# Performance work log

Hardware: AMD Instinct MI355X
Metric: run time of the kernel (lower is better)

## Reference

```python
import jax, jax.numpy as jnp
import numpy as np

EPS = 1e-10

def _quantize_one(x, codebook):
    # x: [B, T, D]; codebook: [K, D]
    B, T, D = x.shape
    K = codebook.shape[0]
    flat = x.reshape(-1, D)  # [N, D]
    # squared euclidean distance (argmin of this == argmax of -dist in torch code)
    dist = (jnp.sum(flat * flat, axis=-1, keepdims=True)
            - 2.0 * flat @ codebook.T
            + jnp.sum(codebook * codebook, axis=-1))  # [N, K]
    ind = jnp.argmin(dist, axis=-1)  # [N]
    q = codebook[ind].reshape(B, T, D)
    # commitment loss: mse(quantize.detach(), x) * commitment(=1.0)
    loss = jnp.mean((jax.lax.stop_gradient(q) - x) ** 2)
    # straight-through estimator
    q_st = x + jax.lax.stop_gradient(q - x)
    # perplexity from one-hot encodings
    counts = jnp.zeros((K,), dtype=x.dtype).at[ind].add(1.0)
    avg_probs = counts / ind.shape[0]
    perplexity = jnp.exp(-jnp.sum(avg_probs * jnp.log(avg_probs + EPS)))
    return q_st, loss, perplexity

def setup_inputs() -> dict:
    key = jax.random.key(0)
    k1, k2 = jax.random.split(key)
    z = jax.random.normal(k1, (16, 64, 4096), dtype=jnp.float32)
    codebooks = jax.random.normal(k2, (8, 1024, 64), dtype=jnp.float32)
    return {"z": z, "codebooks": codebooks}

def reference(z, codebooks):
    # z: [B, code_dim, T] -> transpose(2,1) -> [B, T, code_dim]
    x = jnp.transpose(z, (0, 2, 1))

    def step(carry, cb):
        residual, quantized_out = carry
        q, loss, perp = _quantize_one(residual, cb)
        return (residual - q, quantized_out + q), (loss, perp)

    (_, quantized_out), (losses, perplexities) = jax.lax.scan(
        step, (x, jnp.zeros_like(x)), codebooks)
    zq = jnp.transpose(quantized_out, (0, 2, 1))  # back to [B, code_dim, T]
    return zq, losses, perplexities
```

## Files before the change

kernel.cpp:

```cpp
#include <hip/hip_runtime.h>

#define S      8
#define K      1024
#define D      64
#define NVEC   65536
#define NW     2048
#define NELEM  4194304.0f
#define EPSQ   1e-10f
#define DELTA  0.005f

typedef __attribute__((ext_vector_type(8))) short  short8;
typedef __attribute__((ext_vector_type(4))) float  float4v;

static __device__ inline unsigned short f2bf(float f) {
    unsigned int u = __float_as_uint(f);
    u = (u + 0x7FFFu + ((u >> 16) & 1u)) >> 16;
    return (unsigned short)u;
}
static __device__ inline float bf2f(unsigned short h) {
    return __uint_as_float(((unsigned int)h) << 16);
}

__global__ void rvq_prep(const float* __restrict__ cb,
                         unsigned short* __restrict__ cbi,
                         float* __restrict__ c2, unsigned* __restrict__ cnt) {
    int i = blockIdx.x * blockDim.x + threadIdx.x;
    if (i < S * K) {
        const float* row = cb + (size_t)i * D;
        float a0 = 0.f, a1 = 0.f, a2 = 0.f, a3 = 0.f;
#pragma unroll
        for (int d = 0; d < D; d += 4) {
            a0 = fmaf(row[d+0], row[d+0], a0);
            a1 = fmaf(row[d+1], row[d+1], a1);
            a2 = fmaf(row[d+2], row[d+2], a2);
            a3 = fmaf(row[d+3], row[d+3], a3);
        }
        c2[i] = (a0 + a1) + (a2 + a3);
        cnt[i] = 0u;
    }
    int s  = i >> 12;
    int tau = (i >> 6) & 63;
    int l  = i & 63;
    int m  = l & 15, qq = l >> 4;
    const float* row = cb + (size_t)(s * K + tau * 16 + m) * D;
    short8 h0h, h0l, h1h, h1l;
#pragma unroll
    for (int e = 0; e < 8; ++e) {
        float x = row[qq * 8 + e];
        unsigned short h = f2bf(x);
        h0h[e] = (short)h; h0l[e] = (short)f2bf(x - bf2f(h));
        float y = row[32 + qq * 8 + e];
        unsigned short g = f2bf(y);
        h1h[e] = (short)g; h1l[e] = (short)f2bf(y - bf2f(g));
    }
    unsigned short* rec = cbi + (size_t)(s * 64 + tau) * 2048 + l * 8;
    *(short8*)(rec +    0) = h0h;
    *(short8*)(rec +  512) = h1h;
    *(short8*)(rec + 1024) = h0l;
    *(short8*)(rec + 1536) = h1l;
}

__global__ __launch_bounds__(64, 2)
void rvq_main(const float* __restrict__ z, const float* __restrict__ cbf,
              const unsigned short* __restrict__ cbi,
              const float* __restrict__ c2, float* __restrict__ zq,
              float* __restrict__ lossp, unsigned* __restrict__ cnt) {
    const int lane = threadIdx.x;
    const int m    = lane & 15;
    const int q    = lane >> 4;
    const int wid  = blockIdx.x;
    const int vbase = wid * 32;
    const int b    = vbase >> 12;
    const int ta   = (vbase & 4095) + m;
    const int tb   = ta + 16;
    const size_t zrow = ((size_t)(b * 64)) << 12;

    float ra0[8], ra1[8], rb0[8], rb1[8];
#pragma unroll
    for (int i = 0; i < 8; ++i) {
        ra0[i] = z[zrow + ((size_t)(q*8+i)    << 12) + ta];
        ra1[i] = z[zrow + ((size_t)(32+q*8+i) << 12) + ta];
        rb0[i] = z[zrow + ((size_t)(q*8+i)    << 12) + tb];
        rb1[i] = z[zrow + ((size_t)(32+q*8+i) << 12) + tb];
    }

#define LOADTILE(B0v, B1v, B2v, B3v, CCv, tt) {                              \
        const unsigned short* p_ = recs + (size_t)(tt) * 2048 + lane * 8;    \
        B0v = *(const short8*)(p_);                                          \
        B1v = *(const short8*)(p_ + 512);                                    \
        B2v = *(const short8*)(p_ + 1024);                                   \
        B3v = *(const short8*)(p_ + 1536);                                   \
        CCv = c2s[(tt) * 16 + m]; }

#pragma unroll 1
    for (int s = 0; s < S; ++s) {
        short8 xa0h, xa0l, xa1h, xa1l, xb0h, xb0l, xb1h, xb1l;
#pragma unroll
        for (int i = 0; i < 8; ++i) {
            unsigned short h;
            h = f2bf(ra0[i]); xa0h[i] = (short)h; xa0l[i] = (short)f2bf(ra0[i] - bf2f(h));
            h = f2bf(ra1[i]); xa1h[i] = (short)h; xa1l[i] = (short)f2bf(ra1[i] - bf2f(h));
            h = f2bf(rb0[i]); xb0h[i] = (short)h; xb0l[i] = (short)f2bf(rb0[i] - bf2f(h));
            h = f2bf(rb1[i]); xb1h[i] = (short)h; xb1l[i] = (short)f2bf(rb1[i] - bf2f(h));
        }

        float b1a[4], b2a[4], b1b[4], b2b[4];
        int   k1a[4], k1b[4];
#pragma unroll
        for (int j = 0; j < 4; ++j) {
            b1a[j] = 3.4e38f; b2a[j] = 3.4e38f; k1a[j] = 0;
            b1b[j] = 3.4e38f; b2b[j] = 3.4e38f; k1b[j] = 0;
        }

        const unsigned short* recs = cbi + (size_t)s * 131072;
        const float*          c2s  = c2 + s * K;

        short8 A0, A1, A2, A3, C0, C1, C2, C3;
        float  ca, cb2;
        LOADTILE(A0, A1, A2, A3, ca,  0);
        LOADTILE(C0, C1, C2, C3, cb2, 1);

#pragma unroll 1
        for (int tau = 0; tau < 64; tau += 2) {
            {
                short8 bh0 = A0, bh1 = A1, bl0 = A2, bl1 = A3;
                float  c2v = ca;
                if (tau + 2 < 64) LOADTILE(A0, A1, A2, A3, ca, tau + 2);
                float4v aa = {0.f,0.f,0.f,0.f}, ab = {0.f,0.f,0.f,0.f};
                aa = __builtin_amdgcn_mfma_f32_16x16x32_bf16(xa0h, bh0, aa, 0,0,0);
                aa = __builtin_amdgcn_mfma_f32_16x16x32_bf16(xa0l, bh0, aa, 0,0,0);
                aa = __builtin_amdgcn_mfma_f32_16x16x32_bf16(xa0h, bl0, aa, 0,0,0);
                aa = __builtin_amdgcn_mfma_f32_16x16x32_bf16(xa1h, bh1, aa, 0,0,0);
                aa = __builtin_amdgcn_mfma_f32_16x16x32_bf16(xa1l, bh1, aa, 0,0,0);
                aa = __builtin_amdgcn_mfma_f32_16x16x32_bf16(xa1h, bl1, aa, 0,0,0);
                ab = __builtin_amdgcn_mfma_f32_16x16x32_bf16(xb0h, bh0, ab, 0,0,0);
                ab = __builtin_amdgcn_mfma_f32_16x16x32_bf16(xb0l, bh0, ab, 0,0,0);
                ab = __builtin_amdgcn_mfma_f32_16x16x32_bf16(xb0h, bl0, ab, 0,0,0);
                ab = __builtin_amdgcn_mfma_f32_16x16x32_bf16(xb1h, bh1, ab, 0,0,0);
                ab = __builtin_amdgcn_mfma_f32_16x16x32_bf16(xb1l, bh1, ab, 0,0,0);
                ab = __builtin_amdgcn_mfma_f32_16x16x32_bf16(xb1h, bl1, ab, 0,0,0);
                int ncol = tau * 16 + m;
#pragma unroll
                for (int j = 0; j < 4; ++j) {
                    float sa = fmaf(-2.f, aa[j], c2v);
                    b2a[j] = fminf(b2a[j], fmaxf(sa, b1a[j]));
                    k1a[j] = (sa < b1a[j]) ? ncol : k1a[j];
                    b1a[j] = fminf(sa, b1a[j]);
                    float sb = fmaf(-2.f, ab[j], c2v);
                    b2b[j] = fminf(b2b[j], fmaxf(sb, b1b[j]));
                    k1b[j] = (sb < b1b[j]) ? ncol : k1b[j];
                    b1b[j] = fminf(sb, b1b[j]);
                }
            }
            {
                short8 bh0 = C0, bh1 = C1, bl0 = C2, bl1 = C3;
                float  c2v = cb2;
                if (tau + 3 < 64) LOADTILE(C0, C1, C2, C3, cb2, tau + 3);
                float4v aa = {0.f,0.f,0.f,0.f}, ab = {0.f,0.f,0.f,0.f};
                aa = __builtin_amdgcn_mfma_f32_16x16x32_bf16(xa0h, bh0, aa, 0,0,0);
                aa = __builtin_amdgcn_mfma_f32_16x16x32_bf16(xa0l, bh0, aa, 0,0,0);
                aa = __builtin_amdgcn_mfma_f32_16x16x32_bf16(xa0h, bl0, aa, 0,0,0);
                aa = __builtin_amdgcn_mfma_f32_16x16x32_bf16(xa1h, bh1, aa, 0,0,0);
                aa = __builtin_amdgcn_mfma_f32_16x16x32_bf16(xa1l, bh1, aa, 0,0,0);
                aa = __builtin_amdgcn_mfma_f32_16x16x32_bf16(xa1h, bl1, aa, 0,0,0);
                ab = __builtin_amdgcn_mfma_f32_16x16x32_bf16(xb0h, bh0, ab, 0,0,0);
                ab = __builtin_amdgcn_mfma_f32_16x16x32_bf16(xb0l, bh0, ab, 0,0,0);
                ab = __builtin_amdgcn_mfma_f32_16x16x32_bf16(xb0h, bl0, ab, 0,0,0);
                ab = __builtin_amdgcn_mfma_f32_16x16x32_bf16(xb1h, bh1, ab, 0,0,0);
                ab = __builtin_amdgcn_mfma_f32_16x16x32_bf16(xb1l, bh1, ab, 0,0,0);
                ab = __builtin_amdgcn_mfma_f32_16x16x32_bf16(xb1h, bl1, ab, 0,0,0);
                int ncol = (tau + 1) * 16 + m;
#pragma unroll
                for (int j = 0; j < 4; ++j) {
                    float sa = fmaf(-2.f, aa[j], c2v);
                    b2a[j] = fminf(b2a[j], fmaxf(sa, b1a[j]));
                    k1a[j] = (sa < b1a[j]) ? ncol : k1a[j];
                    b1a[j] = fminf(sa, b1a[j]);
                    float sb = fmaf(-2.f, ab[j], c2v);
                    b2b[j] = fminf(b2b[j], fmaxf(sb, b1b[j]));
                    k1b[j] = (sb < b1b[j]) ? ncol : k1b[j];
                    b1b[j] = fminf(sb, b1b[j]);
                }
            }
        }

#pragma unroll
        for (int off = 1; off < 16; off <<= 1) {
#pragma unroll
            for (int j = 0; j < 4; ++j) {
                float o1 = __shfl_xor(b1a[j], off); int ok = __shfl_xor(k1a[j], off);
                float o2 = __shfl_xor(b2a[j], off);
                float n2 = fminf(fminf(b2a[j], o2), fmaxf(b1a[j], o1));
                bool tk = (o1 < b1a[j]) || (o1 == b1a[j] && ok < k1a[j]);
                k1a[j] = tk ? ok : k1a[j]; b1a[j] = fminf(b1a[j], o1); b2a[j] = n2;
                o1 = __shfl_xor(b1b[j], off); ok = __shfl_xor(k1b[j], off);
                o2 = __shfl_xor(b2b[j], off);
                n2 = fminf(fminf(b2b[j], o2), fmaxf(b1b[j], o1));
                tk = (o1 < b1b[j]) || (o1 == b1b[j] && ok < k1b[j]);
                k1b[j] = tk ? ok : k1b[j]; b1b[j] = fminf(b1b[j], o1); b2b[j] = n2;
            }
        }

        const float* cr0 = cbf + (size_t)s * 65536;
#define RESCUE(b1X, b2X, k1X, R0, R1)                                         \
        for (int j = 0; j < 4; ++j) {                                         \
            unsigned long long mask = __ballot(b2X[j] - b1X[j] < DELTA);      \
            while (mask) {                                                    \
                int lq = (int)(__builtin_ctzll(mask)) >> 4;                   \
                mask &= ~(0xFFFFULL << (lq * 16));                            \
                int mrow = lq * 4 + j;                                        \
                float bd = 3.4e38f; int bk = 0;                               \
                for (int cc = 0; cc < 16; ++cc) {                             \
                    int n = cc * 64 + lane;                                   \
                    const float* crow = cr0 + (size_t)n * 64;                 \
                    float dot = 0.f;                                          \
                    for (int p = 0; p < 4; ++p) {                             \
                        for (int i = 0; i < 8; ++i)                           \
                            dot = fmaf(__shfl(R0[i], mrow + 16*p), crow[p*8+i], dot); \
                        for (int i = 0; i < 8; ++i)                           \
                            dot = fmaf(__shfl(R1[i], mrow + 16*p), crow[32+p*8+i], dot); \
                    }                                                         \
                    float sc = c2s[n] - 2.f * dot;                            \
                    if (sc < bd) { bd = sc; bk = n; }                         \
                }                                                             \
                for (int off = 1; off < 64; off <<= 1) {                      \
                    float ob = __shfl_xor(bd, off); int ok = __shfl_xor(bk, off); \
                    bool tk = (ob < bd) || (ob == bd && ok < bk);             \
                    bk = tk ? ok : bk; bd = fminf(bd, ob);                    \
                }                                                             \
                if (q == lq) k1X[j] = bk;                                     \
            }                                                                 \
        }
        RESCUE(b1a, b2a, k1a, ra0, ra1)
        RESCUE(b1b, b2b, k1b, rb0, rb1)
#undef RESCUE

        int mm = m & 3, src = (m >> 2) * 16;
        int wa0 = __shfl(k1a[0], src), wa1 = __shfl(k1a[1], src);
        int wa2 = __shfl(k1a[2], src), wa3 = __shfl(k1a[3], src);
        int bka = (mm == 0) ? wa0 : (mm == 1) ? wa1 : (mm == 2) ? wa2 : wa3;
        int wb0 = __shfl(k1b[0], src), wb1 = __shfl(k1b[1], src);
        int wb2 = __shfl(k1b[2], src), wb3 = __shfl(k1b[3], src);
        int bkb = (mm == 0) ? wb0 : (mm == 1) ? wb1 : (mm == 2) ? wb2 : wb3;

        const float* qa = cbf + (size_t)s * 65536 + (size_t)bka * 64;
        const float* qb = cbf + (size_t)s * 65536 + (size_t)bkb * 64;
#pragma unroll
        for (int i = 0; i < 8; ++i) {
            ra0[i] -= qa[q*8+i];  ra1[i] -= qa[32+q*8+i];
            rb0[i] -= qb[q*8+i];  rb1[i] -= qb[32+q*8+i];
        }

        float ls = 0.f;
#pragma unroll
        for (int i = 0; i < 8; ++i) {
            ls = fmaf(ra0[i], ra0[i], ls); ls = fmaf(ra1[i], ra1[i], ls);
            ls = fmaf(rb0[i], rb0[i], ls); ls = fmaf(rb1[i], rb1[i], ls);
        }
#pragma unroll
        for (int off = 1; off < 64; off <<= 1) ls += __shfl_xor(ls, off);
        if (lane == 0) lossp[s * NW + wid] = ls;

        if (q == 0) {
            atomicAdd(&cnt[s * K + bka], 1u);
            atomicAdd(&cnt[s * K + bkb], 1u);
        }
    }
#undef LOADTILE

#pragma unroll
    for (int i = 0; i < 8; ++i) {
        size_t a0 = zrow + ((size_t)(q*8+i)    << 12) + ta;
        size_t a1 = zrow + ((size_t)(32+q*8+i) << 12) + ta;
        zq[a0] = z[a0] - ra0[i];
        zq[a1] = z[a1] - ra1[i];
        size_t a2 = zrow + ((size_t)(q*8+i)    << 12) + tb;
        size_t a3 = zrow + ((size_t)(32+q*8+i) << 12) + tb;
        zq[a2] = z[a2] - rb0[i];
        zq[a3] = z[a3] - rb1[i];
    }
}

__global__ void rvq_finalize(const float* __restrict__ lossp,
                             const unsigned* __restrict__ cnt,
                             float* __restrict__ out_loss,
                             float* __restrict__ out_perp) {
    const int s   = blockIdx.x;
    const int tid = threadIdx.x;
    float ent = 0.f, lsum = 0.f;
    for (int i = tid; i < K; i += 256) {
        float p = (float)cnt[s * K + i] * (1.0f / 65536.0f);
        ent += p * logf(p + EPSQ);
    }
    for (int i = tid; i < NW; i += 256) lsum += lossp[s * NW + i];
    __shared__ float redE[4], redL[4];
#pragma unroll
    for (int off = 32; off > 0; off >>= 1) {
        ent  += __shfl_down(ent, off);
        lsum += __shfl_down(lsum, off);
    }
    if ((tid & 63) == 0) { redE[tid >> 6] = ent; redL[tid >> 6] = lsum; }
    __syncthreads();
    if (tid == 0) {
        float te = redE[0] + redE[1] + redE[2] + redE[3];
        float tl = redL[0] + redL[1] + redL[2] + redL[3];
        out_perp[s] = expf(-te);
        out_loss[s] = tl * (1.0f / NELEM);
    }
}

extern "C" void kernel_launch(void* const* d_in, const int* in_sizes, int n_in,
                              void* d_out, int out_size, void* d_ws, size_t ws_size,
                              hipStream_t stream) {
    const float* z  = (const float*)d_in[0];
    const float* cb = (const float*)d_in[1];

    float* zq       = (float*)d_out;
    float* out_loss = zq + 4194304;
    float* out_perp = out_loss + 8;

    char* ws = (char*)d_ws;
    unsigned short* cbi = (unsigned short*)(ws);
    float*    c2    = (float*)(ws + 2097152);
    unsigned* cnt   = (unsigned*)(ws + 2129920);
    float*    lossp = (float*)(ws + 2162688);

    hipLaunchKernelGGL(rvq_prep,     dim3(128),  dim3(256), 0, stream, cb, cbi, c2, cnt);
    hipLaunchKernelGGL(rvq_main,     dim3(NW),   dim3(64),  0, stream, z, cb, cbi, c2, zq, lossp, cnt);
    hipLaunchKernelGGL(rvq_finalize, dim3(S),    dim3(256), 0, stream, lossp, cnt, out_loss, out_perp);
}
```

Measured before the change: 454.7 us.

## Split codebook search across two waves per block with LDS argmin merge

```diff
diff --git a/kernel.cpp b/kernel.cpp
--- a/kernel.cpp
+++ b/kernel.cpp
@@ -4,7 +4,7 @@
 #define K      1024
 #define D      64
 #define NVEC   65536
-#define NW     2048
+#define NB     2048
 #define NELEM  4194304.0f
 #define EPSQ   1e-10f
 #define DELTA  0.005f
@@ -60,12 +60,18 @@
     *(short8*)(rec + 1536) = h1l;
 }
 
-__global__ __launch_bounds__(64, 2)
+__global__ __launch_bounds__(128, 3)
 void rvq_main(const float* __restrict__ z, const float* __restrict__ cbf,
               const unsigned short* __restrict__ cbi,
               const float* __restrict__ c2, float* __restrict__ zq,
               float* __restrict__ lossp, unsigned* __restrict__ cnt) {
-    const int lane = threadIdx.x;
+    __shared__ float lds_b1[2][2][16];
+    __shared__ float lds_b2[2][2][16];
+    __shared__ int   lds_k [2][2][16];
+
+    const int tid  = threadIdx.x;
+    const int lane = tid & 63;
+    const int wave = tid >> 6;
     const int m    = lane & 15;
     const int q    = lane >> 4;
     const int wid  = blockIdx.x;
@@ -74,6 +80,8 @@
     const int ta   = (vbase & 4095) + m;
     const int tb   = ta + 16;
     const size_t zrow = ((size_t)(b * 64)) << 12;
+    const int tbeg = wave * 32;
+    const int tend = tbeg + 32;
 
     float ra0[8], ra1[8], rb0[8], rb1[8];
 #pragma unroll
@@ -117,15 +125,15 @@
 
         short8 A0, A1, A2, A3, C0, C1, C2, C3;
         float  ca, cb2;
-        LOADTILE(A0, A1, A2, A3, ca,  0);
-        LOADTILE(C0, C1, C2, C3, cb2, 1);
+        LOADTILE(A0, A1, A2, A3, ca,  tbeg);
+        LOADTILE(C0, C1, C2, C3, cb2, tbeg + 1);
 
 #pragma unroll 1
-        for (int tau = 0; tau < 64; tau += 2) {
+        for (int tau = tbeg; tau < tend; tau += 2) {
             {
                 short8 bh0 = A0, bh1 = A1, bl0 = A2, bl1 = A3;
                 float  c2v = ca;
-                if (tau + 2 < 64) LOADTILE(A0, A1, A2, A3, ca, tau + 2);
+                if (tau + 2 < tend) LOADTILE(A0, A1, A2, A3, ca, tau + 2);
                 float4v aa = {0.f,0.f,0.f,0.f}, ab = {0.f,0.f,0.f,0.f};
                 aa = __builtin_amdgcn_mfma_f32_16x16x32_bf16(xa0h, bh0, aa, 0,0,0);
                 aa = __builtin_amdgcn_mfma_f32_16x16x32_bf16(xa0l, bh0, aa, 0,0,0);
@@ -155,7 +163,7 @@
             {
                 short8 bh0 = C0, bh1 = C1, bl0 = C2, bl1 = C3;
                 float  c2v = cb2;
-                if (tau + 3 < 64) LOADTILE(C0, C1, C2, C3, cb2, tau + 3);
+                if (tau + 3 < tend) LOADTILE(C0, C1, C2, C3, cb2, tau + 3);
                 float4v aa = {0.f,0.f,0.f,0.f}, ab = {0.f,0.f,0.f,0.f};
                 aa = __builtin_amdgcn_mfma_f32_16x16x32_bf16(xa0h, bh0, aa, 0,0,0);
                 aa = __builtin_amdgcn_mfma_f32_16x16x32_bf16(xa0l, bh0, aa, 0,0,0);
@@ -200,6 +208,30 @@
                 k1b[j] = tk ? ok : k1b[j]; b1b[j] = fminf(b1b[j], o1); b2b[j] = n2;
             }
         }
+
+        if (m == 0) {
+#pragma unroll
+            for (int j = 0; j < 4; ++j) {
+                lds_b1[wave][0][q*4+j] = b1a[j]; lds_b2[wave][0][q*4+j] = b2a[j]; lds_k[wave][0][q*4+j] = k1a[j];
+                lds_b1[wave][1][q*4+j] = b1b[j]; lds_b2[wave][1][q*4+j] = b2b[j]; lds_k[wave][1][q*4+j] = k1b[j];
+            }
+        }
+        __syncthreads();
+        {
+            int ow = 1 - wave;
+#pragma unroll
+            for (int j = 0; j < 4; ++j) {
+                float o1 = lds_b1[ow][0][q*4+j]; float o2 = lds_b2[ow][0][q*4+j]; int ok = lds_k[ow][0][q*4+j];
+                float n2 = fminf(fminf(b2a[j], o2), fmaxf(b1a[j], o1));
+                bool tk = (o1 < b1a[j]) || (o1 == b1a[j] && ok < k1a[j]);
+                k1a[j] = tk ? ok : k1a[j]; b1a[j] = fminf(b1a[j], o1); b2a[j] = n2;
+                o1 = lds_b1[ow][1][q*4+j]; o2 = lds_b2[ow][1][q*4+j]; ok = lds_k[ow][1][q*4+j];
+                n2 = fminf(fminf(b2b[j], o2), fmaxf(b1b[j], o1));
+                tk = (o1 < b1b[j]) || (o1 == b1b[j] && ok < k1b[j]);
+                k1b[j] = tk ? ok : k1b[j]; b1b[j] = fminf(b1b[j], o1); b2b[j] = n2;
+            }
+        }
+        __syncthreads();
 
         const float* cr0 = cbf + (size_t)s * 65536;
 #define RESCUE(b1X, b2X, k1X, R0, R1)                                         \
@@ -251,33 +283,36 @@
             rb0[i] -= qb[q*8+i];  rb1[i] -= qb[32+q*8+i];
         }
 
-        float ls = 0.f;
+        if (wave == 0) {
+            float ls = 0.f;
+#pragma unroll
+            for (int i = 0; i < 8; ++i) {
+                ls = fmaf(ra0[i], ra0[i], ls); ls = fmaf(ra1[i], ra1[i], ls);
+                ls = fmaf(rb0[i], rb0[i], ls); ls = fmaf(rb1[i], rb1[i], ls);
+            }
+#pragma unroll
+            for (int off = 1; off < 64; off <<= 1) ls += __shfl_xor(ls, off);
+            if (lane == 0) lossp[s * NB + wid] = ls;
+            if (q == 0) {
+                atomicAdd(&cnt[s * K + bka], 1u);
+                atomicAdd(&cnt[s * K + bkb], 1u);
+            }
+        }
+    }
+#undef LOADTILE
+
+    if (wave == 0) {
 #pragma unroll
         for (int i = 0; i < 8; ++i) {
-            ls = fmaf(ra0[i], ra0[i], ls); ls = fmaf(ra1[i], ra1[i], ls);
-            ls = fmaf(rb0[i], rb0[i], ls); ls = fmaf(rb1[i], rb1[i], ls);
-        }
-#pragma unroll
-        for (int off = 1; off < 64; off <<= 1) ls += __shfl_xor(ls, off);
-        if (lane == 0) lossp[s * NW + wid] = ls;
-
-        if (q == 0) {
-            atomicAdd(&cnt[s * K + bka], 1u);
-            atomicAdd(&cnt[s * K + bkb], 1u);
-        }
-    }
-#undef LOADTILE
-
-#pragma unroll
-    for (int i = 0; i < 8; ++i) {
-        size_t a0 = zrow + ((size_t)(q*8+i)    << 12) + ta;
-        size_t a1 = zrow + ((size_t)(32+q*8+i) << 12) + ta;
-        zq[a0] = z[a0] - ra0[i];
-        zq[a1] = z[a1] - ra1[i];
-        size_t a2 = zrow + ((size_t)(q*8+i)    << 12) + tb;
-        size_t a3 = zrow + ((size_t)(32+q*8+i) << 12) + tb;
-        zq[a2] = z[a2] - rb0[i];
-        zq[a3] = z[a3] - rb1[i];
+            size_t a0 = zrow + ((size_t)(q*8+i)    << 12) + ta;
+            size_t a1 = zrow + ((size_t)(32+q*8+i) << 12) + ta;
+            zq[a0] = z[a0] - ra0[i];
+            zq[a1] = z[a1] - ra1[i];
+            size_t a2 = zrow + ((size_t)(q*8+i)    << 12) + tb;
+            size_t a3 = zrow + ((size_t)(32+q*8+i) << 12) + tb;
+            zq[a2] = z[a2] - rb0[i];
+            zq[a3] = z[a3] - rb1[i];
+        }
     }
 }
 
@@ -292,7 +327,7 @@
         float p = (float)cnt[s * K + i] * (1.0f / 65536.0f);
         ent += p * logf(p + EPSQ);
     }
-    for (int i = tid; i < NW; i += 256) lsum += lossp[s * NW + i];
+    for (int i = tid; i < NB; i += 256) lsum += lossp[s * NB + i];
     __shared__ float redE[4], redL[4];
 #pragma unroll
     for (int off = 32; off > 0; off >>= 1) {
@@ -326,6 +361,6 @@
     float*    lossp = (float*)(ws + 2162688);
 
     hipLaunchKernelGGL(rvq_prep,     dim3(128),  dim3(256), 0, stream, cb, cbi, c2, cnt);
-    hipLaunchKernelGGL(rvq_main,     dim3(NW),   dim3(64),  0, stream, z, cb, cbi, c2, zq, lossp, cnt);
+    hipLaunchKernelGGL(rvq_main,     dim3(NB),   dim3(128), 0, stream, z, cb, cbi, c2, zq, lossp, cnt);
     hipLaunchKernelGGL(rvq_finalize, dim3(S),    dim3(256), 0, stream, lossp, cnt, out_loss, out_perp);
 }
```

New measurement: 1.123 ms. +147.1%, slower.
